# Kernel tuning notes

Hardware: AMD Instinct MI355X
Metric: run time of the kernel (lower is better)

## Reference

```python
import jax, jax.numpy as jnp
import numpy as np

EPS_NORM = 1e-12   # torch F.normalize eps
EPS_BN = 1e-5      # BatchNorm1d eps
NEG_SLOPE = 0.01   # LeakyReLU default


def _l2_normalize(x, axis):
    # torch F.normalize: x / max(||x||, eps)
    n = jnp.sqrt(jnp.sum(x * x, axis=axis, keepdims=True))
    return x / jnp.maximum(n, EPS_NORM)


def setup_inputs() -> dict:
    key = jax.random.key(0)
    k1, k2, k3, k4, k5, k6, k7 = jax.random.split(key, 7)
    B, C, N, M, OUT = 8, 128, 4096, 4096, 128
    return {
        "input": jax.random.normal(k1, (B, C, N), dtype=jnp.float32),
        "target_g": jax.random.normal(k2, (B, C, M), dtype=jnp.float32),
        "weight": jax.random.normal(k3, (C, OUT), dtype=jnp.float32) * (1.0 / np.sqrt(OUT)),
        "gamma": jax.random.normal(k4, (OUT,), dtype=jnp.float32),
        "beta": jax.random.normal(k5, (OUT,), dtype=jnp.float32),
        "running_mean": jax.random.normal(k6, (OUT,), dtype=jnp.float32),
        "running_var": jax.random.uniform(k7, (OUT,), dtype=jnp.float32, minval=0.5, maxval=1.5),
    }


def reference(input, target_g, weight, gamma, beta, running_mean, running_var):
    # input: [B, C, N], target_g: [B, C, M]
    # cosine-similarity adjacency: [B, M, N]
    tg = _l2_normalize(target_g, axis=1)
    inp_n = _l2_normalize(input, axis=1)
    adj = jnp.einsum('bcm,bcn->bmn', tg, inp_n)
    adj = jax.nn.softmax(adj, axis=-1)
    # aggregate: [B, M, C]
    agg = jnp.einsum('bmn,bcn->bmc', adj, input)
    # project: [B, M, OUT] -> permute to [B, OUT, M]
    out = jnp.einsum('bmc,co->bom', agg, weight)
    # LeakyReLU then BatchNorm1d (eval mode, running stats)
    out = jnp.where(out >= 0, out, NEG_SLOPE * out)
    inv = jax.lax.rsqrt(running_var + EPS_BN)
    out = (out - running_mean[None, :, None]) * (inv * gamma)[None, :, None] + beta[None, :, None]
    return out
```

## Files before the change

### kernel.cpp

```cpp
#include <hip/hip_runtime.h>
#include <hip/hip_bf16.h>

#define BATCH 8
#define CDIM 128
#define NDIM 4096

typedef __bf16 bf16x8 __attribute__((ext_vector_type(8)));
typedef float f32x4 __attribute__((ext_vector_type(4)));
typedef float f32x16 __attribute__((ext_vector_type(16)));
typedef unsigned u32x4 __attribute__((ext_vector_type(4)));

#define QT_OFF 0u
#define KT_OFF 8388608u
#define VB_OFF 16777216u
#define WT_OFF 25165824u
#define SC_OFF (WT_OFF + 32768u)
#define BI_OFF (SC_OFF + 512u)

__device__ __forceinline__ f32x4 mfma16(bf16x8 a, bf16x8 b, f32x4 c) {
    return __builtin_amdgcn_mfma_f32_16x16x32_bf16(a, b, c, 0, 0, 0);
}
__device__ __forceinline__ f32x16 mfma32(bf16x8 a, bf16x8 b, f32x16 c) {
    return __builtin_amdgcn_mfma_f32_32x32x16_bf16(a, b, c, 0, 0, 0);
}

__device__ __forceinline__ unsigned pack2bf(float a, float b) {
    unsigned short ul = __builtin_bit_cast(unsigned short, (__bf16)a);
    unsigned short uh = __builtin_bit_cast(unsigned short, (__bf16)b);
    return (unsigned)ul | ((unsigned)uh << 16);
}

__device__ __forceinline__ void glds16(const void* g, void* l) {
    __builtin_amdgcn_global_load_lds((__attribute__((address_space(1))) void*)(void*)g,
                                     (__attribute__((address_space(3))) void*)l, 16, 0, 0);
}

__global__ __launch_bounds__(256) void prep_nt(const float* __restrict__ input,
                                               const float* __restrict__ tg,
                                               const float* __restrict__ wgt,
                                               const float* __restrict__ gamma,
                                               const float* __restrict__ beta,
                                               const float* __restrict__ mean,
                                               const float* __restrict__ var,
                                               void* __restrict__ ws) {
    __shared__ float Tt[64][129];
    __shared__ float psum[4][64];
    __shared__ float rn[64];
    const int n0 = blockIdx.x * 64;
    const int b  = blockIdx.y;
    const int tid = threadIdx.x;
    const float* src = (blockIdx.z == 0 ? input : tg) + (size_t)b * CDIM * NDIM;

    #pragma unroll
    for (int i = 0; i < 8; ++i) {
        int f = tid + i * 256;
        int c = f >> 4, j4 = f & 15;
        float4 v = *(const float4*)(src + (size_t)c * NDIM + n0 + j4 * 4);
        Tt[j4 * 4 + 0][c] = v.x;
        Tt[j4 * 4 + 1][c] = v.y;
        Tt[j4 * 4 + 2][c] = v.z;
        Tt[j4 * 4 + 3][c] = v.w;
    }
    __syncthreads();
    {
        int j = tid & 63, part = tid >> 6;
        float ss = 0.f;
        #pragma unroll 8
        for (int c = part * 32; c < part * 32 + 32; ++c) { float x = Tt[j][c]; ss += x * x; }
        psum[part][j] = ss;
    }
    __syncthreads();
    if (tid < 64) {
        float s = psum[0][tid] + psum[1][tid] + psum[2][tid] + psum[3][tid];
        rn[tid] = 1.0f / fmaxf(sqrtf(s), 1e-12f);
    }
    __syncthreads();

    __hip_bfloat16* dstT = (__hip_bfloat16*)((char*)ws + (blockIdx.z == 0 ? KT_OFF : QT_OFF))
                           + ((size_t)b * NDIM + n0) * CDIM;
    #pragma unroll
    for (int i = 0; i < 8; ++i) {
        int f = tid + i * 256;
        int j = f >> 5, c4 = f & 31;
        float r = rn[j];
        float4 v = *(const float4*)&Tt[j][c4 * 4];
        uint2 pk; pk.x = pack2bf(v.x * r, v.y * r); pk.y = pack2bf(v.z * r, v.w * r);
        *(uint2*)((unsigned short*)dstT + (size_t)j * CDIM + c4 * 4) = pk;
    }
    if (blockIdx.z == 0) {
        __hip_bfloat16* vb = (__hip_bfloat16*)((char*)ws + VB_OFF) + (size_t)b * CDIM * NDIM + n0;
        #pragma unroll
        for (int i = 0; i < 8; ++i) {
            int f = tid + i * 256;
            int c = f >> 4, j4 = f & 15;
            float x0 = Tt[j4 * 4 + 0][c], x1 = Tt[j4 * 4 + 1][c];
            float x2 = Tt[j4 * 4 + 2][c], x3 = Tt[j4 * 4 + 3][c];
            uint2 pv; pv.x = pack2bf(x0, x1); pv.y = pack2bf(x2, x3);
            *(uint2*)((unsigned short*)vb + (size_t)c * NDIM + j4 * 4) = pv;
        }
    } else if (blockIdx.x == 0 && b == 0) {
        __hip_bfloat16* wT = (__hip_bfloat16*)((char*)ws + WT_OFF);
        float* sc = (float*)((char*)ws + SC_OFF);
        float* bi = (float*)((char*)ws + BI_OFF);
        #pragma unroll
        for (int i = 0; i < 64; ++i) {
            int f = tid + i * 256;
            int c = f >> 7, o = f & 127;
            wT[o * 128 + c] = __hip_bfloat16(wgt[c * 128 + o]);
        }
        if (tid < 128) {
            float inv = rsqrtf(var[tid] + 1e-5f);
            float s = inv * gamma[tid];
            sc[tid] = s;
            bi[tid] = beta[tid] - mean[tid] * s;
        }
    }
}

__global__ __launch_bounds__(512, 2) void flash5(const void* __restrict__ ws_,
                                                 float* __restrict__ out) {
    extern __shared__ char smem[];
    const char* ws = (const char*)ws_;
    const __hip_bfloat16* Qt = (const __hip_bfloat16*)(ws + QT_OFF);
    const __hip_bfloat16* Kt = (const __hip_bfloat16*)(ws + KT_OFF);
    const __hip_bfloat16* Vb = (const __hip_bfloat16*)(ws + VB_OFF);
    const __hip_bfloat16* wT = (const __hip_bfloat16*)(ws + WT_OFF);
    const float* scale = (const float*)(ws + SC_OFF);
    const float* bias  = (const float*)(ws + BI_OFF);

    const int bx = blockIdx.x;
    const int b  = bx & 7;
    const int m0 = (bx >> 3) * 128;
    const int tid = threadIdx.x;
    const int w = tid >> 6, lane = tid & 63;
    const int hf = lane >> 5;
    const int l31 = lane & 31;
    const int nt = w & 1;
    const int mt = w >> 1;

    const char* kgb = (const char*)(Kt + (size_t)b * NDIM * CDIM);
    const char* vgb = (const char*)(Vb + (size_t)b * CDIM * NDIM);

    bf16x8 qb[8];
    {
        const char* qrow = (const char*)Qt + ((size_t)b * NDIM + m0 + mt * 32 + l31) * 256 + hf * 16;
        #pragma unroll
        for (int s = 0; s < 8; ++s) qb[s] = *(const bf16x8*)(qrow + s * 32);
    }

    unsigned kOff[8];
    {
        int nn = nt * 32 + l31;
        #pragma unroll
        for (int s = 0; s < 8; ++s)
            kOff[s] = nn * 256 + (((2 * s + hf) ^ (nn & 15)) * 16);
    }
    unsigned vOff[2][4];
    #pragma unroll
    for (int t = 0; t < 2; ++t)
        #pragma unroll
        for (int ca = 0; ca < 4; ++ca) {
            int c = ca * 32 + l31;
            vOff[t][ca] = 16384 + c * 128 + (((nt * 4 + t * 2 + hf) ^ (c & 7)) * 16);
        }

    const char* kSrc[2]; const char* vSrc[2];
    unsigned kDst[2], vDst[2];
    #pragma unroll
    for (int i = 0; i < 2; ++i) {
        int slot = i * 512 + tid;
        int n = slot >> 4, j = slot & 15;
        kSrc[i] = kgb + n * 256 + ((j ^ (n & 15)) * 16);
        kDst[i] = i * 8192 + w * 1024;
        int c = slot >> 3, j8 = slot & 7;
        vSrc[i] = vgb + (size_t)c * 8192 + ((j8 ^ (c & 7)) * 16);
        vDst[i] = 16384 + i * 8192 + w * 1024;
    }

    f32x16 oacc[4];
    #pragma unroll
    for (int ca = 0; ca < 4; ++ca)
        #pragma unroll
        for (int i = 0; i < 16; ++i) oacc[ca][i] = 0.f;
    float lacc = 0.f;

    #pragma unroll
    for (int i = 0; i < 2; ++i) { glds16(kSrc[i], smem + kDst[i]); kSrc[i] += 16384; }
    #pragma unroll
    for (int i = 0; i < 2; ++i) { glds16(vSrc[i], smem + vDst[i]); vSrc[i] += 128; }

    auto body = [&](const unsigned bo, const bool do_pref) {
        asm volatile("s_waitcnt vmcnt(0) lgkmcnt(0)\ns_barrier" ::: "memory");
        if (do_pref) {
            const unsigned obo = bo ^ 32768u;
            #pragma unroll
            for (int i = 0; i < 2; ++i) { glds16(kSrc[i], smem + (obo + kDst[i])); kSrc[i] += 16384; }
            #pragma unroll
            for (int i = 0; i < 2; ++i) { glds16(vSrc[i], smem + (obo + vDst[i])); vSrc[i] += 128; }
        }

        f32x16 st;
        #pragma unroll
        for (int i = 0; i < 16; ++i) st[i] = 0.f;
        #pragma unroll
        for (int s = 0; s < 8; ++s) {
            bf16x8 kf = *(const bf16x8*)(smem + bo + kOff[s]);
            st = mfma32(kf, qb[s], st);
        }

        unsigned d[8];
        float lsum = 0.f;
        #pragma unroll
        for (int rq = 0; rq < 4; ++rq) {
            float e0 = __expf(st[rq * 4 + 0] - 1.0f);
            float e1 = __expf(st[rq * 4 + 1] - 1.0f);
            float e2 = __expf(st[rq * 4 + 2] - 1.0f);
            float e3 = __expf(st[rq * 4 + 3] - 1.0f);
            lsum += (e0 + e1) + (e2 + e3);
            d[rq * 2 + 0] = pack2bf(e0, e1);
            d[rq * 2 + 1] = pack2bf(e2, e3);
        }
        lacc += lsum;
        unsigned o[8];
        #pragma unroll
        for (int j = 0; j < 8; ++j) o[j] = (unsigned)__shfl_xor((int)d[j], 32, 64);
        bf16x8 pf[2];
        #pragma unroll
        for (int t = 0; t < 2; ++t) {
            u32x4 tv;
            tv.x = hf ? o[4 * t + 2] : d[4 * t + 0];
            tv.y = hf ? o[4 * t + 3] : d[4 * t + 1];
            tv.z = hf ? d[4 * t + 2] : o[4 * t + 0];
            tv.w = hf ? d[4 * t + 3] : o[4 * t + 1];
            pf[t] = __builtin_bit_cast(bf16x8, tv);
        }

        #pragma unroll
        for (int t = 0; t < 2; ++t) {
            #pragma unroll
            for (int ca = 0; ca < 4; ++ca) {
                bf16x8 vf = *(const bf16x8*)(smem + bo + vOff[t][ca]);
                oacc[ca] = mfma32(vf, pf[t], oacc[ca]);
            }
        }
    };

    for (int ii = 0; ii < 32; ++ii) {
        body(0u, true);
        body(32768u, ii != 31);
    }

    float lw = lacc + __shfl_xor(lacc, 32, 64);
    __syncthreads();
    float* lLds = (float*)(smem + 65536);
    if (lane < 32) lLds[w * 32 + lane] = lw;
    if (w & 1) {
        float4* dst = (float4*)smem + (w >> 1) * 1024 + lane;
        #pragma unroll
        for (int ca = 0; ca < 4; ++ca)
            #pragma unroll
            for (int rq = 0; rq < 4; ++rq) {
                float4 t = { oacc[ca][rq * 4 + 0], oacc[ca][rq * 4 + 1],
                             oacc[ca][rq * 4 + 2], oacc[ca][rq * 4 + 3] };
                dst[(ca * 4 + rq) * 64] = t;
            }
    }
    __syncthreads();
    char* sAgg = smem + 67584;
    if (!(w & 1)) {
        float linv = 1.0f / (lLds[w * 32 + l31] + lLds[(w + 1) * 32 + l31]);
        const float4* srcp = (const float4*)smem + (w >> 1) * 1024 + lane;
        int m = (w >> 1) * 32 + l31;
        char* aggRow = sAgg + m * 256;
        const int mx = (m & 7) << 1;
        #pragma unroll
        for (int ca = 0; ca < 4; ++ca)
            #pragma unroll
            for (int rq = 0; rq < 4; ++rq) {
                float4 ov = srcp[(ca * 4 + rq) * 64];
                float v0 = (oacc[ca][rq * 4 + 0] + ov.x) * linv;
                float v1 = (oacc[ca][rq * 4 + 1] + ov.y) * linv;
                float v2 = (oacc[ca][rq * 4 + 2] + ov.z) * linv;
                float v3 = (oacc[ca][rq * 4 + 3] + ov.w) * linv;
                int cq = ca * 8 + rq * 2 + hf;
                uint2 pk; pk.x = pack2bf(v0, v1); pk.y = pack2bf(v2, v3);
                *(uint2*)(aggRow + ((cq ^ mx) * 8)) = pk;
            }
    }
    __syncthreads();

    const int li = lane & 15, q = lane >> 4;
    const int pm = w * 16 + li;
    f32x4 racc[8];
    #pragma unroll
    for (int ob = 0; ob < 8; ++ob) { racc[ob][0]=0.f; racc[ob][1]=0.f; racc[ob][2]=0.f; racc[ob][3]=0.f; }
    #pragma unroll
    for (int ks = 0; ks < 4; ++ks) {
        int slot8 = ((ks * 4 + q) * 2) ^ ((li & 7) << 1);
        bf16x8 af = *(const bf16x8*)(sAgg + pm * 256 + slot8 * 8);
        #pragma unroll
        for (int ob = 0; ob < 8; ++ob) {
            bf16x8 wf = *(const bf16x8*)((const char*)wT + (ob * 16 + li) * 256 + ks * 64 + q * 16);
            racc[ob] = mfma16(af, wf, racc[ob]);
        }
    }

    float* sRes = (float*)smem;
    #pragma unroll
    for (int ob = 0; ob < 8; ++ob) {
        int oo = ob * 16 + li;
        float sc = scale[oo], bi = bias[oo];
        #pragma unroll
        for (int r = 0; r < 4; ++r) {
            float v = racc[ob][r];
            v = (v >= 0.0f) ? v : 0.01f * v;
            v = v * sc + bi;
            sRes[oo * 132 + w * 16 + q * 4 + r] = v;
        }
    }
    __syncthreads();

    float* outb = out + (size_t)b * CDIM * NDIM + m0;
    #pragma unroll
    for (int i = 0; i < 8; ++i) {
        int f = tid + i * 512;
        int o = f >> 5, mq = f & 31;
        *(float4*)(outb + (size_t)o * NDIM + mq * 4) = *(const float4*)(sRes + o * 132 + mq * 4);
    }
}

extern "C" void kernel_launch(void* const* d_in, const int* in_sizes, int n_in,
                              void* d_out, int out_size, void* d_ws, size_t ws_size,
                              hipStream_t stream) {
    const float* input  = (const float*)d_in[0];
    const float* tg     = (const float*)d_in[1];
    const float* weight = (const float*)d_in[2];
    const float* gamma  = (const float*)d_in[3];
    const float* beta   = (const float*)d_in[4];
    const float* rmean  = (const float*)d_in[5];
    const float* rvar   = (const float*)d_in[6];
    float* out = (float*)d_out;

    (void)in_sizes; (void)n_in; (void)out_size; (void)ws_size;

    hipFuncSetAttribute(reinterpret_cast<const void*>(flash5),
                        hipFuncAttributeMaxDynamicSharedMemorySize, 100352);

    dim3 gprep(NDIM / 64, BATCH, 2);
    prep_nt<<<gprep, 256, 0, stream>>>(input, tg, weight, gamma, beta, rmean, rvar, d_ws);
    flash5<<<dim3(256), 512, 100352, stream>>>(d_ws, out);
}
```

Before: 190.4 us.

## Double the key tile per stage and fold log2e into query normalization

Each pipeline stage now loads 128 keys instead of 64 into a 128KB double-buffered LDS, so the loop has half as many iterations and barriers. Each stage runs two score blocks and interleaves softmax with the PV MFMAs. The log2(e) factor is folded into the normalized query during prep, so exp becomes exp2 without a subtract. The final epilogue writes float4 results straight to global memory instead of staging a transpose through LDS. The larger LDS footprint may reduce blocks per CU, and the direct stores are less coalesced.

```diff
diff --git a/kernel.cpp b/kernel.cpp
--- a/kernel.cpp
+++ b/kernel.cpp
@@ -50,6 +50,7 @@
     const int b  = blockIdx.y;
     const int tid = threadIdx.x;
     const float* src = (blockIdx.z == 0 ? input : tg) + (size_t)b * CDIM * NDIM;
+    const float zscale = (blockIdx.z == 0) ? 1.0f : 1.44269504f;
 
     #pragma unroll
     for (int i = 0; i < 8; ++i) {
@@ -82,7 +83,7 @@
     for (int i = 0; i < 8; ++i) {
         int f = tid + i * 256;
         int j = f >> 5, c4 = f & 31;
-        float r = rn[j];
+        float r = rn[j] * zscale;
         float4 v = *(const float4*)&Tt[j][c4 * 4];
         uint2 pk; pk.x = pack2bf(v.x * r, v.y * r); pk.y = pack2bf(v.z * r, v.w * r);
         *(uint2*)((unsigned short*)dstT + (size_t)j * CDIM + c4 * 4) = pk;
@@ -117,7 +118,7 @@
     }
 }
 
-__global__ __launch_bounds__(512, 2) void flash5(const void* __restrict__ ws_,
+__global__ __launch_bounds__(512, 2) void flash6(const void* __restrict__ ws_,
                                                  float* __restrict__ out) {
     extern __shared__ char smem[];
     const char* ws = (const char*)ws_;
@@ -161,21 +162,15 @@
         #pragma unroll
         for (int ca = 0; ca < 4; ++ca) {
             int c = ca * 32 + l31;
-            vOff[t][ca] = 16384 + c * 128 + (((nt * 4 + t * 2 + hf) ^ (c & 7)) * 16);
-        }
-
-    const char* kSrc[2]; const char* vSrc[2];
-    unsigned kDst[2], vDst[2];
-    #pragma unroll
-    for (int i = 0; i < 2; ++i) {
-        int slot = i * 512 + tid;
-        int n = slot >> 4, j = slot & 15;
-        kSrc[i] = kgb + n * 256 + ((j ^ (n & 15)) * 16);
-        kDst[i] = i * 8192 + w * 1024;
-        int c = slot >> 3, j8 = slot & 7;
-        vSrc[i] = vgb + (size_t)c * 8192 + ((j8 ^ (c & 7)) * 16);
-        vDst[i] = 16384 + i * 8192 + w * 1024;
-    }
+            vOff[t][ca] = 32768 + c * 256 + (((nt * 4 + t * 2 + hf) ^ (c & 15)) * 16);
+        }
+
+    const int t4 = tid >> 4, j16 = tid & 15;
+    const int swz = j16 ^ (t4 & 15);
+    const char* kSrcP = kgb + t4 * 256 + swz * 16;
+    const char* vSrcP = vgb + (size_t)t4 * 8192 + swz * 16;
+    const unsigned kDstB = w * 1024;
+    const unsigned vDstB = 32768 + w * 1024;
 
     f32x16 oacc[4];
     #pragma unroll
@@ -185,37 +180,20 @@
     float lacc = 0.f;
 
     #pragma unroll
-    for (int i = 0; i < 2; ++i) { glds16(kSrc[i], smem + kDst[i]); kSrc[i] += 16384; }
-    #pragma unroll
-    for (int i = 0; i < 2; ++i) { glds16(vSrc[i], smem + vDst[i]); vSrc[i] += 128; }
-
-    auto body = [&](const unsigned bo, const bool do_pref) {
-        asm volatile("s_waitcnt vmcnt(0) lgkmcnt(0)\ns_barrier" ::: "memory");
-        if (do_pref) {
-            const unsigned obo = bo ^ 32768u;
-            #pragma unroll
-            for (int i = 0; i < 2; ++i) { glds16(kSrc[i], smem + (obo + kDst[i])); kSrc[i] += 16384; }
-            #pragma unroll
-            for (int i = 0; i < 2; ++i) { glds16(vSrc[i], smem + (obo + vDst[i])); vSrc[i] += 128; }
-        }
-
-        f32x16 st;
-        #pragma unroll
-        for (int i = 0; i < 16; ++i) st[i] = 0.f;
-        #pragma unroll
-        for (int s = 0; s < 8; ++s) {
-            bf16x8 kf = *(const bf16x8*)(smem + bo + kOff[s]);
-            st = mfma32(kf, qb[s], st);
-        }
-
+    for (int i = 0; i < 4; ++i) glds16(kSrcP + i * 8192, smem + kDstB + i * 8192);
+    #pragma unroll
+    for (int i = 0; i < 4; ++i) glds16(vSrcP + (size_t)i * 262144, smem + vDstB + i * 8192);
+    kSrcP += 32768; vSrcP += 256;
+
+    auto make_pf = [&](const f32x16& st, bf16x8 pf[2]) {
         unsigned d[8];
         float lsum = 0.f;
         #pragma unroll
         for (int rq = 0; rq < 4; ++rq) {
-            float e0 = __expf(st[rq * 4 + 0] - 1.0f);
-            float e1 = __expf(st[rq * 4 + 1] - 1.0f);
-            float e2 = __expf(st[rq * 4 + 2] - 1.0f);
-            float e3 = __expf(st[rq * 4 + 3] - 1.0f);
+            float e0 = exp2f(st[rq * 4 + 0]);
+            float e1 = exp2f(st[rq * 4 + 1]);
+            float e2 = exp2f(st[rq * 4 + 2]);
+            float e3 = exp2f(st[rq * 4 + 3]);
             lsum += (e0 + e1) + (e2 + e3);
             d[rq * 2 + 0] = pack2bf(e0, e1);
             d[rq * 2 + 1] = pack2bf(e2, e3);
@@ -224,7 +202,6 @@
         unsigned o[8];
         #pragma unroll
         for (int j = 0; j < 8; ++j) o[j] = (unsigned)__shfl_xor((int)d[j], 32, 64);
-        bf16x8 pf[2];
         #pragma unroll
         for (int t = 0; t < 2; ++t) {
             u32x4 tv;
@@ -234,50 +211,89 @@
             tv.w = hf ? d[4 * t + 3] : o[4 * t + 1];
             pf[t] = __builtin_bit_cast(bf16x8, tv);
         }
-
-        #pragma unroll
-        for (int t = 0; t < 2; ++t) {
+    };
+
+    auto body = [&](const unsigned bo, const bool do_pref) {
+        asm volatile("s_waitcnt vmcnt(0) lgkmcnt(0)\ns_barrier" ::: "memory");
+        if (do_pref) {
+            const unsigned obo = bo ^ 65536u;
+            #pragma unroll
+            for (int i = 0; i < 4; ++i)
+                glds16(kSrcP + i * 8192, smem + obo + kDstB + i * 8192);
+            #pragma unroll
+            for (int i = 0; i < 4; ++i)
+                glds16(vSrcP + (size_t)i * 262144, smem + obo + vDstB + i * 8192);
+            kSrcP += 32768; vSrcP += 256;
+        }
+
+        f32x16 st0, st1;
+        #pragma unroll
+        for (int i = 0; i < 16; ++i) { st0[i] = 0.f; st1[i] = 0.f; }
+        #pragma unroll
+        for (int s = 0; s < 8; ++s) {
+            bf16x8 kf = *(const bf16x8*)(smem + bo + kOff[s]);
+            st0 = mfma32(kf, qb[s], st0);
+        }
+        #pragma unroll
+        for (int s = 0; s < 8; ++s) {
+            bf16x8 kf = *(const bf16x8*)(smem + bo + 16384 + kOff[s]);
+            st1 = mfma32(kf, qb[s], st1);
+        }
+
+        bf16x8 pf0[2];
+        make_pf(st0, pf0);
+        #pragma unroll
+        for (int t = 0; t < 2; ++t)
             #pragma unroll
             for (int ca = 0; ca < 4; ++ca) {
                 bf16x8 vf = *(const bf16x8*)(smem + bo + vOff[t][ca]);
-                oacc[ca] = mfma32(vf, pf[t], oacc[ca]);
+                oacc[ca] = mfma32(vf, pf0[t], oacc[ca]);
             }
-        }
+
+        bf16x8 pf1[2];
+        make_pf(st1, pf1);
+        #pragma unroll
+        for (int t = 0; t < 2; ++t)
+            #pragma unroll
+            for (int ca = 0; ca < 4; ++ca) {
+                bf16x8 vf = *(const bf16x8*)(smem + bo + (vOff[t][ca] ^ 128u));
+                oacc[ca] = mfma32(vf, pf1[t], oacc[ca]);
+            }
     };
 
-    for (int ii = 0; ii < 32; ++ii) {
+    for (int ii = 0; ii < 16; ++ii) {
         body(0u, true);
-        body(32768u, ii != 31);
+        body(65536u, ii != 15);
     }
 
     float lw = lacc + __shfl_xor(lacc, 32, 64);
     __syncthreads();
-    float* lLds = (float*)(smem + 65536);
-    if (lane < 32) lLds[w * 32 + lane] = lw;
-    if (w & 1) {
-        float4* dst = (float4*)smem + (w >> 1) * 1024 + lane;
+    char* slab = smem + mt * 16512;
+    if (nt == 1) {
+        float4* dst = (float4*)slab;
         #pragma unroll
         for (int ca = 0; ca < 4; ++ca)
             #pragma unroll
             for (int rq = 0; rq < 4; ++rq) {
                 float4 t = { oacc[ca][rq * 4 + 0], oacc[ca][rq * 4 + 1],
                              oacc[ca][rq * 4 + 2], oacc[ca][rq * 4 + 3] };
-                dst[(ca * 4 + rq) * 64] = t;
+                dst[(ca * 4 + rq) * 64 + lane] = t;
             }
-    }
-    __syncthreads();
-    char* sAgg = smem + 67584;
-    if (!(w & 1)) {
-        float linv = 1.0f / (lLds[w * 32 + l31] + lLds[(w + 1) * 32 + l31]);
-        const float4* srcp = (const float4*)smem + (w >> 1) * 1024 + lane;
-        int m = (w >> 1) * 32 + l31;
+        if (lane < 32) ((float*)(slab + 16384))[l31] = lw;
+    }
+    __syncthreads();
+    char* sAgg = smem + 66560;
+    if (nt == 0) {
+        float linv = 1.0f / (lw + ((const float*)(slab + 16384))[l31]);
+        const float4* srcp = (const float4*)slab;
+        int m = mt * 32 + l31;
         char* aggRow = sAgg + m * 256;
         const int mx = (m & 7) << 1;
         #pragma unroll
         for (int ca = 0; ca < 4; ++ca)
             #pragma unroll
             for (int rq = 0; rq < 4; ++rq) {
-                float4 ov = srcp[(ca * 4 + rq) * 64];
+                float4 ov = srcp[(ca * 4 + rq) * 64 + lane];
                 float v0 = (oacc[ca][rq * 4 + 0] + ov.x) * linv;
                 float v1 = (oacc[ca][rq * 4 + 1] + ov.y) * linv;
                 float v2 = (oacc[ca][rq * 4 + 2] + ov.z) * linv;
@@ -305,27 +321,17 @@
         }
     }
 
-    float* sRes = (float*)smem;
+    float* outb = out + (size_t)b * CDIM * NDIM + m0 + w * 16;
     #pragma unroll
     for (int ob = 0; ob < 8; ++ob) {
-        int oo = ob * 16 + li;
-        float sc = scale[oo], bi = bias[oo];
-        #pragma unroll
-        for (int r = 0; r < 4; ++r) {
-            float v = racc[ob][r];
-            v = (v >= 0.0f) ? v : 0.01f * v;
-            v = v * sc + bi;
-            sRes[oo * 132 + w * 16 + q * 4 + r] = v;
-        }
-    }
-    __syncthreads();
-
-    float* outb = out + (size_t)b * CDIM * NDIM + m0;
-    #pragma unroll
-    for (int i = 0; i < 8; ++i) {
-        int f = tid + i * 512;
-        int o = f >> 5, mq = f & 31;
-        *(float4*)(outb + (size_t)o * NDIM + mq * 4) = *(const float4*)(sRes + o * 132 + mq * 4);
+        int o = ob * 16 + li;
+        float sc = scale[o], bi = bias[o];
+        float4 vst;
+        float v0 = racc[ob][0]; v0 = (v0 >= 0.f) ? v0 : 0.01f * v0; vst.x = v0 * sc + bi;
+        float v1 = racc[ob][1]; v1 = (v1 >= 0.f) ? v1 : 0.01f * v1; vst.y = v1 * sc + bi;
+        float v2 = racc[ob][2]; v2 = (v2 >= 0.f) ? v2 : 0.01f * v2; vst.z = v2 * sc + bi;
+        float v3 = racc[ob][3]; v3 = (v3 >= 0.f) ? v3 : 0.01f * v3; vst.w = v3 * sc + bi;
+        *(float4*)(outb + (size_t)o * NDIM + q * 4) = vst;
     }
 }
 
@@ -343,10 +349,10 @@
 
     (void)in_sizes; (void)n_in; (void)out_size; (void)ws_size;
 
-    hipFuncSetAttribute(reinterpret_cast<const void*>(flash5),
-                        hipFuncAttributeMaxDynamicSharedMemorySize, 100352);
+    hipFuncSetAttribute(reinterpret_cast<const void*>(flash6),
+                        hipFuncAttributeMaxDynamicSharedMemorySize, 131072);
 
     dim3 gprep(NDIM / 64, BATCH, 2);
     prep_nt<<<gprep, 256, 0, stream>>>(input, tg, weight, gamma, beta, rmean, rvar, d_ws);
-    flash5<<<dim3(256), 512, 100352, stream>>>(d_ws, out);
-}
+    flash6<<<dim3(256), 512, 131072, stream>>>(d_ws, out);
+}
```

After: 195.4 us. 1.03x slower.
